# Kernel optimization log

Hardware: AMD Instinct MI355X
Metric: run time of the kernel (lower is better)

Reference implementation:

```python
import jax, jax.numpy as jnp
import numpy as np

B, T, C = 4, 2048, 1024

def setup_inputs() -> dict:
    key = jax.random.key(0)
    kx, kq, kk, kv = jax.random.split(key, 4)
    s = C ** -0.5  # match nn.Linear init scale roughly
    return {
        "x": jax.random.normal(kx, (B, T, C), dtype=jnp.float32),
        "Wq": jax.random.normal(kq, (C, C), dtype=jnp.float32) * s,
        "Wk": jax.random.normal(kk, (C, C), dtype=jnp.float32) * s,
        "Wv": jax.random.normal(kv, (C, C), dtype=jnp.float32) * s,
    }

def reference(x, Wq, Wk, Wv):
    Bq, Tq, Cq = x.shape
    # nn.Linear: y = x @ W^T (bias=False)
    q = jnp.einsum('btc,dc->btd', x, Wq)
    k = jnp.einsum('btc,dc->btd', x, Wk)
    v = jnp.einsum('btc,dc->btd', x, Wv)
    scale = Cq ** -0.5
    qk = jnp.einsum('btd,bsd->bts', q, k) * scale  # [B, T, T]
    causal = jnp.tril(jnp.ones((Tq, Tq), dtype=bool))
    qk = jnp.where(causal, qk, -jnp.inf)
    attn = jax.nn.softmax(qk, axis=-1)
    out = jnp.einsum('bts,bsd->btd', attn, v)
    return out
```

## Files before the change

kernel.cpp:

```cpp
#include <hip/hip_runtime.h>
#include <hip/hip_fp16.h>


typedef __attribute__((ext_vector_type(8))) _Float16 half8;
typedef __attribute__((ext_vector_type(4))) _Float16 half4;
typedef __attribute__((ext_vector_type(4))) float f32x4;

template<int TM, int TN, int WM, int WN, bool SWAP>
__device__ __forceinline__ void gemm_nt_core(
    const _Float16* __restrict__ A, const _Float16* __restrict__ B,
    int lda, int ldb, int k0, int k1,
    _Float16* ldsA, _Float16* ldsB,
    f32x4 acc[TM / (WM * 16)][TN / (WN * 16)])
{
    constexpr int FM = TM / (WM * 16), FN = TN / (WN * 16);
    constexpr int NA = TM / 32, NB = TN / 32;
    const int t    = threadIdx.x;
    const int lane = t & 63;
    const int w    = t >> 6;
    const int wm   = w % WM;
    const int wn   = w / WM;
    const int lr   = lane & 15;
    const int lq   = lane >> 4;

    const _Float16* ga[NA]; int loA[NA];
    const _Float16* gb[NB]; int loB[NB];
#pragma unroll
    for (int i = 0; i < NA; ++i) {
        int f = t + 256 * i;
        int r = f >> 3, c = (f & 7) ^ ((f >> 3) & 7);
        ga[i] = A + (size_t)r * lda + c * 8;
        loA[i] = f * 8;
    }
#pragma unroll
    for (int i = 0; i < NB; ++i) {
        int f = t + 256 * i;
        int r = f >> 3, c = (f & 7) ^ ((f >> 3) & 7);
        gb[i] = B + (size_t)r * ldb + c * 8;
        loB[i] = f * 8;
    }

    int offA[2][FM], offB[2][FN];
#pragma unroll
    for (int h = 0; h < 2; ++h) {
#pragma unroll
        for (int i = 0; i < FM; ++i) {
            int R = wm * (TM / WM) + i * 16 + lr;
            offA[h][i] = (8 * R + ((h * 4 + lq) ^ (R & 7))) * 8;
        }
#pragma unroll
        for (int i = 0; i < FN; ++i) {
            int R = wn * (TN / WN) + i * 16 + lr;
            offB[h][i] = (8 * R + ((h * 4 + lq) ^ (R & 7))) * 8;
        }
    }

    half8 va[NA], vb[NB];
#pragma unroll
    for (int i = 0; i < NA; ++i) va[i] = *(const half8*)(ga[i] + k0);
#pragma unroll
    for (int i = 0; i < NB; ++i) vb[i] = *(const half8*)(gb[i] + k0);

    for (int k = k0; k < k1; k += 64) {
        __syncthreads();
#pragma unroll
        for (int i = 0; i < NA; ++i) *(half8*)(ldsA + loA[i]) = va[i];
#pragma unroll
        for (int i = 0; i < NB; ++i) *(half8*)(ldsB + loB[i]) = vb[i];
        if (k + 64 < k1) {
#pragma unroll
            for (int i = 0; i < NA; ++i) va[i] = *(const half8*)(ga[i] + k + 64);
#pragma unroll
            for (int i = 0; i < NB; ++i) vb[i] = *(const half8*)(gb[i] + k + 64);
        }
        __syncthreads();

#pragma unroll
        for (int h = 0; h < 2; ++h) {
            half8 af[FM], bf[FN];
#pragma unroll
            for (int i = 0; i < FM; ++i) af[i] = *(const half8*)(ldsA + offA[h][i]);
#pragma unroll
            for (int i = 0; i < FN; ++i) bf[i] = *(const half8*)(ldsB + offB[h][i]);
#pragma unroll
            for (int mi = 0; mi < FM; ++mi)
#pragma unroll
                for (int ni = 0; ni < FN; ++ni) {
                    if constexpr (SWAP)
                        acc[mi][ni] = __builtin_amdgcn_mfma_f32_16x16x32_f16(
                            bf[ni], af[mi], acc[mi][ni], 0, 0, 0);
                    else
                        acc[mi][ni] = __builtin_amdgcn_mfma_f32_16x16x32_f16(
                            af[mi], bf[ni], acc[mi][ni], 0, 0, 0);
                }
        }
    }
}

__global__ __launch_bounds__(256) void f32tof16_k(
    const float* __restrict__ in, _Float16* __restrict__ out, int n)
{
    int i = (blockIdx.x * 256 + threadIdx.x) * 4;
    if (i < n) {
        float4 f = *(const float4*)(in + i);
        half4 h = { (_Float16)f.x, (_Float16)f.y, (_Float16)f.z, (_Float16)f.w };
        *(half4*)(out + i) = h;
    }
}

__global__ __launch_bounds__(256) void wconv_k(
    const float* __restrict__ Wq, const float* __restrict__ Wk,
    const float* __restrict__ Wv, _Float16* __restrict__ out)
{
    const float* src = (blockIdx.y == 0) ? Wq : (blockIdx.y == 1) ? Wk : Wv;
    int i = (blockIdx.x * 256 + threadIdx.x) * 4;
    float4 f = *(const float4*)(src + i);
    half4 h = { (_Float16)f.x, (_Float16)f.y, (_Float16)f.z, (_Float16)f.w };
    *(half4*)(out + (size_t)blockIdx.y * 1024 * 1024 + i) = h;
}

__global__ __launch_bounds__(256) void qkv_gemm_k(
    const _Float16* __restrict__ xh, const _Float16* __restrict__ Wh,
    _Float16* __restrict__ Q, _Float16* __restrict__ K, _Float16* __restrict__ Vt)
{
    __shared__ __align__(16) _Float16 ldsA[128 * 64];
    __shared__ __align__(16) _Float16 ldsB[128 * 64];
    const int tileM = blockIdx.x * 128;
    const int tileN = blockIdx.y * 128;
    const int z     = blockIdx.z;
    const _Float16* W = Wh + (size_t)z * 1024 * 1024;

    const int lane = threadIdx.x & 63;
    const int w    = threadIdx.x >> 6;
    const int wm = w & 1, wn = w >> 1;
    const int lr = lane & 15, lq = lane >> 4;

    if (z == 2) {
        f32x4 acc[4][4] = {};
        gemm_nt_core<128, 128, 2, 2, false>(xh + (size_t)tileM * 1024,
                                            W + (size_t)tileN * 1024,
                                            1024, 1024, 0, 1024, ldsA, ldsB, acc);
#pragma unroll
        for (int mi = 0; mi < 4; ++mi)
#pragma unroll
            for (int ni = 0; ni < 4; ++ni) {
                int m0 = tileM + wm * 64 + mi * 16 + lq * 4;
                int n  = tileN + wn * 64 + ni * 16 + lr;
                int b = m0 >> 11, tt = m0 & 2047;
                half4 h = { (_Float16)acc[mi][ni][0], (_Float16)acc[mi][ni][1],
                            (_Float16)acc[mi][ni][2], (_Float16)acc[mi][ni][3] };
                *(half4*)(Vt + (size_t)b * 2048 * 1024 + (size_t)n * 2048 + tt) = h;
            }
    } else {
        f32x4 acc[4][4] = {};
        gemm_nt_core<128, 128, 2, 2, true>(xh + (size_t)tileM * 1024,
                                           W + (size_t)tileN * 1024,
                                           1024, 1024, 0, 1024, ldsA, ldsB, acc);
        _Float16* O = (z == 0) ? Q : K;
#pragma unroll
        for (int mi = 0; mi < 4; ++mi)
#pragma unroll
            for (int ni = 0; ni < 4; ++ni) {
                int tt = tileM + wm * 64 + mi * 16 + lr;
                int d0 = tileN + wn * 64 + ni * 16 + lq * 4;
                half4 h = { (_Float16)acc[mi][ni][0], (_Float16)acc[mi][ni][1],
                            (_Float16)acc[mi][ni][2], (_Float16)acc[mi][ni][3] };
                *(half4*)(O + (size_t)tt * 1024 + d0) = h;
            }
    }
}

__global__ __launch_bounds__(256) void scores_gemm_k(
    const _Float16* __restrict__ Q, const _Float16* __restrict__ K,
    _Float16* __restrict__ S)
{
    const int ti = blockIdx.x, si = blockIdx.y;
    if (si > ti) return;
    const int tileT = ti * 128, tileS = si * 128, b = blockIdx.z;

    __shared__ __align__(16) _Float16 ldsA[128 * 64];
    __shared__ __align__(16) _Float16 ldsB[128 * 64];
    f32x4 acc[4][4] = {};
    gemm_nt_core<128, 128, 2, 2, true>(
        Q + (size_t)b * 2048 * 1024 + (size_t)tileT * 1024,
        K + (size_t)b * 2048 * 1024 + (size_t)tileS * 1024,
        1024, 1024, 0, 1024, ldsA, ldsB, acc);

    const int lane = threadIdx.x & 63;
    const int w    = threadIdx.x >> 6;
    const int wm = w & 1, wn = w >> 1;
    const int lr = lane & 15, lq = lane >> 4;
    const float scale = 0.03125f;

#pragma unroll
    for (int mi = 0; mi < 4; ++mi)
#pragma unroll
        for (int ni = 0; ni < 4; ++ni) {
            int tt = tileT + wm * 64 + mi * 16 + lr;
            int s0 = tileS + wn * 64 + ni * 16 + lq * 4;
            half4 h;
#pragma unroll
            for (int r = 0; r < 4; ++r)
                h[r] = (s0 + r <= tt) ? (_Float16)(acc[mi][ni][r] * scale)
                                      : (_Float16)0.f;
            *(half4*)(S + ((size_t)b * 2048 + tt) * 2048 + s0) = h;
        }
}

__global__ __launch_bounds__(256) void softmax_k(_Float16* __restrict__ S)
{
    const int w    = threadIdx.x >> 6;
    const int lane = threadIdx.x & 63;
    const int t    = blockIdx.x * 4 + w;
    const int b    = blockIdx.y;
    _Float16* row = S + ((size_t)b * 2048 + t) * 2048;

    float x[32];
    float mx = -1e30f;
#pragma unroll
    for (int j = 0; j < 4; ++j) {
        half8 h = *(const half8*)(row + j * 512 + lane * 8);
#pragma unroll
        for (int e = 0; e < 8; ++e) {
            int s = j * 512 + lane * 8 + e;
            float f = (s <= t) ? (float)h[e] : -1e30f;
            x[j * 8 + e] = f;
            mx = fmaxf(mx, f);
        }
    }
#pragma unroll
    for (int o = 32; o > 0; o >>= 1) mx = fmaxf(mx, __shfl_xor(mx, o));

    float sum = 0.f;
#pragma unroll
    for (int i = 0; i < 32; ++i) {
        float e = __expf(x[i] - mx);
        x[i] = e;
        sum += e;
    }
#pragma unroll
    for (int o = 32; o > 0; o >>= 1) sum += __shfl_xor(sum, o);
    const float inv = 1.0f / sum;

#pragma unroll
    for (int j = 0; j < 4; ++j) {
        half8 p;
#pragma unroll
        for (int e = 0; e < 8; ++e) p[e] = (_Float16)(x[j * 8 + e] * inv);
        *(half8*)(row + j * 512 + lane * 8) = p;
    }
}

__global__ __launch_bounds__(256) void pv_gemm_k(
    const _Float16* __restrict__ P, const _Float16* __restrict__ Vt,
    float* __restrict__ out)
{
    __shared__ __align__(16) _Float16 ldsA[128 * 64];
    __shared__ __align__(16) _Float16 ldsB[64 * 64];
    const int tileT = (15 - blockIdx.x) * 128;
    const int tileD = blockIdx.y * 64;
    const int b     = blockIdx.z;
    const int kEnd  = tileT + 128;

    f32x4 acc[4][2] = {};
    gemm_nt_core<128, 64, 2, 2, true>(
        P + ((size_t)b * 2048 + tileT) * 2048,
        Vt + (size_t)b * 1024 * 2048 + (size_t)tileD * 2048,
        2048, 2048, 0, kEnd, ldsA, ldsB, acc);

    const int lane = threadIdx.x & 63;
    const int w    = threadIdx.x >> 6;
    const int wm = w & 1, wn = w >> 1;
    const int lr = lane & 15, lq = lane >> 4;

#pragma unroll
    for (int mi = 0; mi < 4; ++mi)
#pragma unroll
        for (int ni = 0; ni < 2; ++ni) {
            int tt = tileT + wm * 64 + mi * 16 + lr;
            int d0 = tileD + wn * 32 + ni * 16 + lq * 4;
            *(f32x4*)(out + ((size_t)b * 2048 + tt) * 1024 + d0) = acc[mi][ni];
        }
}

extern "C" void kernel_launch(void* const* d_in, const int* in_sizes, int n_in,
                              void* d_out, int out_size, void* d_ws, size_t ws_size,
                              hipStream_t stream)
{
    const float* x  = (const float*)d_in[0];
    const float* Wq = (const float*)d_in[1];
    const float* Wk = (const float*)d_in[2];
    const float* Wv = (const float*)d_in[3];
    float* out = (float*)d_out;

    char* ws = (char*)d_ws;
    _Float16* xh = (_Float16*)(ws);
    _Float16* Wh = (_Float16*)(ws + (16u << 20));
    _Float16* Qh = (_Float16*)(ws + (22u << 20));
    _Float16* Kh = (_Float16*)(ws + (38u << 20));
    _Float16* Vt = (_Float16*)(ws + (54u << 20));
    _Float16* S  = (_Float16*)(ws + (70u << 20));

    f32tof16_k<<<8192, 256, 0, stream>>>(x, xh, 4 * 2048 * 1024);
    wconv_k<<<dim3(1024, 3), 256, 0, stream>>>(Wq, Wk, Wv, Wh);

    qkv_gemm_k<<<dim3(64, 8, 3), 256, 0, stream>>>(xh, Wh, Qh, Kh, Vt);

    scores_gemm_k<<<dim3(16, 16, 4), 256, 0, stream>>>(Qh, Kh, S);
    softmax_k<<<dim3(512, 4), 256, 0, stream>>>(S);
    pv_gemm_k<<<dim3(16, 16, 4), 256, 0, stream>>>(S, Vt, out);
}
```

Baseline: 266.5 us.

## Rewrite QKV projection as 256x256 pipelined GEMM with direct global-to-LDS loads

Replaces the 128x128 QKV projection GEMM with a 256x256-tile, 512-thread kernel. Operands are streamed directly into swizzled LDS with global_load_lds, double-buffered, and the MFMA work is split into four phases per k-tile interleaved with prefetches and priority hints. The aim is more reuse per tile and hiding of global memory latency behind MFMA work. The cost is 128KB of LDS per block and far fewer blocks (384). The hand-written waitcnt and barrier choreography is fragile.

Measured after the change: 267.2 us. No clear change (+0.3%).

```diff
diff --git a/kernel.cpp b/kernel.cpp
--- a/kernel.cpp
+++ b/kernel.cpp
@@ -97,6 +97,161 @@
     }
 }
 
+__device__ __forceinline__ void gload_lds16(const void* g, void* l)
+{
+    __builtin_amdgcn_global_load_lds(
+        (const __attribute__((address_space(1))) void*)g,
+        (__attribute__((address_space(3))) void*)l, 16, 0, 0);
+}
+
+template<bool SWAP>
+__device__ __forceinline__ void gemm_nt_256(
+    const _Float16* __restrict__ A, const _Float16* __restrict__ B,
+    const int lda, const int ldb, const int kTiles,
+    _Float16* lds, f32x4 acc[8][4])
+{
+    const int t    = threadIdx.x;
+    const int lane = t & 63;
+    const int w    = t >> 6;
+    const int wm   = w & 1;
+    const int wn   = w >> 1;
+    const int lr   = lane & 15;
+    const int lq   = lane >> 4;
+
+    const int r0 = t >> 3;
+    const int c0 = (t & 7) ^ (r0 & 7);
+    const _Float16* gA = A + (size_t)r0 * lda + c0 * 8;
+    const _Float16* gB = B + (size_t)r0 * ldb + c0 * 8;
+
+    char* ldsc = (char*)lds;
+    char* stA = ldsc + w * 1024;
+    char* stB = ldsc + 65536 + w * 1024;
+
+    const int x0 = ((0 + lq) ^ (lr & 7)) * 16;
+    const int x1 = ((4 + lq) ^ (lr & 7)) * 16;
+    const char* rdA = ldsc + wm * 16384 + lr * 128;
+    const char* rdB = ldsc + 65536 + (wn >> 1) * 16384 + (wn & 1) * 8192
+                      + lr * 128;
+
+    half8 af[4][2], bf0[2][2], bf1[2][2];
+
+#define STGA(BUF, H, KOFF) do {                                               \
+    const _Float16* _s = gA + (size_t)(H) * 128 * lda + (KOFF);               \
+    char* _d = stA + (BUF) * 32768 + (H) * 16384;                             \
+    gload_lds16(_s, _d);                                                      \
+    gload_lds16(_s + (size_t)64 * lda, _d + 8192);                            \
+} while (0)
+
+#define STGB(BUF, H, KOFF) do {                                               \
+    const _Float16* _s = gB + (size_t)(H) * 128 * ldb + (KOFF);               \
+    char* _d = stB + (BUF) * 32768 + (H) * 16384;                             \
+    gload_lds16(_s, _d);                                                      \
+    gload_lds16(_s + (size_t)64 * ldb, _d + 8192);                            \
+} while (0)
+
+#define LDA_Q(BUF, MQ) do {                                                   \
+    const char* _p = rdA + (BUF) * 32768 + (MQ) * 8192;                       \
+    _Pragma("unroll")                                                         \
+    for (int mi = 0; mi < 4; ++mi) {                                          \
+        af[mi][0] = *(const half8*)(_p + mi * 2048 + x0);                     \
+        af[mi][1] = *(const half8*)(_p + mi * 2048 + x1);                     \
+    }                                                                         \
+} while (0)
+
+#define LDB_Q(DST, BUF, NQ) do {                                              \
+    const char* _p = rdB + (BUF) * 32768 + (NQ) * 4096;                       \
+    _Pragma("unroll")                                                         \
+    for (int ni = 0; ni < 2; ++ni) {                                          \
+        DST[ni][0] = *(const half8*)(_p + ni * 2048 + x0);                    \
+        DST[ni][1] = *(const half8*)(_p + ni * 2048 + x1);                    \
+    }                                                                         \
+} while (0)
+
+#define MFMA_Q(MQ, NQ, BSRC) do {                                             \
+    _Pragma("unroll")                                                         \
+    for (int mi = 0; mi < 4; ++mi)                                            \
+    _Pragma("unroll")                                                         \
+    for (int ni = 0; ni < 2; ++ni)                                            \
+    _Pragma("unroll")                                                         \
+    for (int kh = 0; kh < 2; ++kh) {                                          \
+        if constexpr (SWAP)                                                   \
+            acc[(MQ)*4+mi][(NQ)*2+ni] = __builtin_amdgcn_mfma_f32_16x16x32_f16(\
+                BSRC[ni][kh], af[mi][kh], acc[(MQ)*4+mi][(NQ)*2+ni], 0, 0, 0);\
+        else                                                                  \
+            acc[(MQ)*4+mi][(NQ)*2+ni] = __builtin_amdgcn_mfma_f32_16x16x32_f16(\
+                af[mi][kh], BSRC[ni][kh], acc[(MQ)*4+mi][(NQ)*2+ni], 0, 0, 0);\
+    }                                                                         \
+} while (0)
+
+#define PH_PRE() do {                                                         \
+    asm volatile("" ::: "memory");                                            \
+    __builtin_amdgcn_s_barrier();                                             \
+    asm volatile("s_waitcnt lgkmcnt(0)" ::: "memory");                        \
+    __builtin_amdgcn_sched_barrier(0);                                        \
+    __builtin_amdgcn_s_setprio(1);                                            \
+} while (0)
+
+#define PH_POST() do {                                                        \
+    __builtin_amdgcn_s_setprio(0);                                            \
+    __builtin_amdgcn_sched_barrier(0);                                        \
+    __builtin_amdgcn_s_barrier();                                             \
+    asm volatile("" ::: "memory");                                            \
+} while (0)
+
+#define KTILE(KT, BUF) do {                                                   \
+    const int _k1 = ((KT) + 1) * 64, _k2 = ((KT) + 2) * 64;                   \
+    const bool _s1 = (KT) + 1 < kTiles, _s2 = (KT) + 2 < kTiles;              \
+                                                                      \
+    LDA_Q(BUF, 0);                                                            \
+    LDB_Q(bf0, BUF, 0);                                                       \
+    if (_s1) STGA((BUF) ^ 1, 1, _k1);                                         \
+    PH_PRE(); MFMA_Q(0, 0, bf0); PH_POST();                                   \
+                                                                      \
+    LDB_Q(bf1, BUF, 1);                                                       \
+    if (_s1) STGB((BUF) ^ 1, 1, _k1);                                         \
+    PH_PRE(); MFMA_Q(0, 1, bf1); PH_POST();                                   \
+                                                                      \
+    LDA_Q(BUF, 1);                                                            \
+    if (_s2) STGB(BUF, 0, _k2);                                               \
+    PH_PRE(); MFMA_Q(1, 1, bf1); PH_POST();                                   \
+                                     \
+    if (_s2) STGA(BUF, 0, _k2);                                               \
+    asm volatile("" ::: "memory");                                            \
+    __builtin_amdgcn_s_barrier();                                             \
+    __builtin_amdgcn_s_setprio(1);                                            \
+    MFMA_Q(1, 0, bf0);                                                        \
+    __builtin_amdgcn_s_setprio(0);                                            \
+    if (_s2) asm volatile("s_waitcnt vmcnt(4)" ::: "memory");                 \
+    else     asm volatile("s_waitcnt vmcnt(0)" ::: "memory");                 \
+    __builtin_amdgcn_sched_barrier(0);                                        \
+    __builtin_amdgcn_s_barrier();                                             \
+    asm volatile("" ::: "memory");                                            \
+} while (0)
+
+    STGA(0, 0, 0); STGA(0, 1, 0); STGB(0, 0, 0); STGB(0, 1, 0);
+    if (kTiles > 1) { STGB(1, 0, 64); STGA(1, 0, 64); }
+    if (kTiles > 1) asm volatile("s_waitcnt vmcnt(4)" ::: "memory");
+    else            asm volatile("s_waitcnt vmcnt(0)" ::: "memory");
+    __builtin_amdgcn_sched_barrier(0);
+    __builtin_amdgcn_s_barrier();
+    asm volatile("" ::: "memory");
+
+#pragma unroll 1
+    for (int kt = 0; kt < kTiles; kt += 2) {
+        KTILE(kt, 0);
+        KTILE(kt + 1, 1);
+    }
+
+#undef STGA
+#undef STGB
+#undef LDA_Q
+#undef LDB_Q
+#undef MFMA_Q
+#undef PH_PRE
+#undef PH_POST
+#undef KTILE
+}
+
 __global__ __launch_bounds__(256) void f32tof16_k(
     const float* __restrict__ in, _Float16* __restrict__ out, int n)
 {
@@ -119,14 +274,14 @@
     *(half4*)(out + (size_t)blockIdx.y * 1024 * 1024 + i) = h;
 }
 
-__global__ __launch_bounds__(256) void qkv_gemm_k(
+__global__ __launch_bounds__(512, 2) void qkv_gemm256_k(
     const _Float16* __restrict__ xh, const _Float16* __restrict__ Wh,
-    _Float16* __restrict__ Q, _Float16* __restrict__ K, _Float16* __restrict__ Vt)
-{
-    __shared__ __align__(16) _Float16 ldsA[128 * 64];
-    __shared__ __align__(16) _Float16 ldsB[128 * 64];
-    const int tileM = blockIdx.x * 128;
-    const int tileN = blockIdx.y * 128;
+    _Float16* __restrict__ Q, _Float16* __restrict__ K,
+    _Float16* __restrict__ Vt)
+{
+    __shared__ __align__(16) _Float16 lds[65536];
+    const int tileM = blockIdx.x * 256;
+    const int tileN = blockIdx.y * 256;
     const int z     = blockIdx.z;
     const _Float16* W = Wh + (size_t)z * 1024 * 1024;
 
@@ -135,16 +290,15 @@
     const int wm = w & 1, wn = w >> 1;
     const int lr = lane & 15, lq = lane >> 4;
 
+    f32x4 acc[8][4] = {};
     if (z == 2) {
-        f32x4 acc[4][4] = {};
-        gemm_nt_core<128, 128, 2, 2, false>(xh + (size_t)tileM * 1024,
-                                            W + (size_t)tileN * 1024,
-                                            1024, 1024, 0, 1024, ldsA, ldsB, acc);
-#pragma unroll
-        for (int mi = 0; mi < 4; ++mi)
+        gemm_nt_256<false>(xh + (size_t)tileM * 1024, W + (size_t)tileN * 1024,
+                           1024, 1024, 16, lds, acc);
+#pragma unroll
+        for (int mi = 0; mi < 8; ++mi)
 #pragma unroll
             for (int ni = 0; ni < 4; ++ni) {
-                int m0 = tileM + wm * 64 + mi * 16 + lq * 4;
+                int m0 = tileM + wm * 128 + mi * 16 + lq * 4;
                 int n  = tileN + wn * 64 + ni * 16 + lr;
                 int b = m0 >> 11, tt = m0 & 2047;
                 half4 h = { (_Float16)acc[mi][ni][0], (_Float16)acc[mi][ni][1],
@@ -152,16 +306,14 @@
                 *(half4*)(Vt + (size_t)b * 2048 * 1024 + (size_t)n * 2048 + tt) = h;
             }
     } else {
-        f32x4 acc[4][4] = {};
-        gemm_nt_core<128, 128, 2, 2, true>(xh + (size_t)tileM * 1024,
-                                           W + (size_t)tileN * 1024,
-                                           1024, 1024, 0, 1024, ldsA, ldsB, acc);
+        gemm_nt_256<true>(xh + (size_t)tileM * 1024, W + (size_t)tileN * 1024,
+                          1024, 1024, 16, lds, acc);
         _Float16* O = (z == 0) ? Q : K;
 #pragma unroll
-        for (int mi = 0; mi < 4; ++mi)
+        for (int mi = 0; mi < 8; ++mi)
 #pragma unroll
             for (int ni = 0; ni < 4; ++ni) {
-                int tt = tileM + wm * 64 + mi * 16 + lr;
+                int tt = tileM + wm * 128 + mi * 16 + lr;
                 int d0 = tileN + wn * 64 + ni * 16 + lq * 4;
                 half4 h = { (_Float16)acc[mi][ni][0], (_Float16)acc[mi][ni][1],
                             (_Float16)acc[mi][ni][2], (_Float16)acc[mi][ni][3] };
@@ -304,7 +456,7 @@
     f32tof16_k<<<8192, 256, 0, stream>>>(x, xh, 4 * 2048 * 1024);
     wconv_k<<<dim3(1024, 3), 256, 0, stream>>>(Wq, Wk, Wv, Wh);
 
-    qkv_gemm_k<<<dim3(64, 8, 3), 256, 0, stream>>>(xh, Wh, Qh, Kh, Vt);
+    qkv_gemm256_k<<<dim3(32, 4, 3), 512, 0, stream>>>(xh, Wh, Qh, Kh, Vt);
 
     scores_gemm_k<<<dim3(16, 16, 4), 256, 0, stream>>>(Qh, Kh, S);
     softmax_k<<<dim3(512, 4), 256, 0, stream>>>(S);
```

## Load GEMM tiles directly into LDS and skip masked softmax chunks

Applied to the files above, without the earlier changes.

Global-to-LDS tile loads in the shared GEMM core now use the direct global_load_lds path instead of staging through registers. This removes the register-prefetch double buffering, so loads are no longer overlapped with the previous tile's MFMA work. Softmax now skips loading, exponentiating and storing 512-column chunks that lie entirely past the causal boundary. Launch bounds request 4 blocks per CU for the GEMM kernels, which caps registers per thread.

New measurement: 302.4 us. +13.5%, slower.

```diff
diff --git a/kernel.cpp b/kernel.cpp
--- a/kernel.cpp
+++ b/kernel.cpp
@@ -6,73 +6,69 @@
 typedef __attribute__((ext_vector_type(4))) _Float16 half4;
 typedef __attribute__((ext_vector_type(4))) float f32x4;
 
-template<int TM, int TN, int WM, int WN, bool SWAP>
-__device__ __forceinline__ void gemm_nt_core(
+__device__ __forceinline__ void gload_lds16(const void* g, void* l)
+{
+    __builtin_amdgcn_global_load_lds(
+        (const __attribute__((address_space(1))) void*)g,
+        (__attribute__((address_space(3))) void*)l, 16, 0, 0);
+}
+
+template<int TM, int TN, bool SWAP>
+__device__ __forceinline__ void gemm_nt_gl(
     const _Float16* __restrict__ A, const _Float16* __restrict__ B,
     int lda, int ldb, int k0, int k1,
     _Float16* ldsA, _Float16* ldsB,
-    f32x4 acc[TM / (WM * 16)][TN / (WN * 16)])
-{
-    constexpr int FM = TM / (WM * 16), FN = TN / (WN * 16);
+    f32x4 acc[TM / 32][TN / 32])
+{
+    constexpr int FM = TM / 32, FN = TN / 32;
     constexpr int NA = TM / 32, NB = TN / 32;
     const int t    = threadIdx.x;
     const int lane = t & 63;
     const int w    = t >> 6;
-    const int wm   = w % WM;
-    const int wn   = w / WM;
+    const int wm   = w & 1;
+    const int wn   = w >> 1;
     const int lr   = lane & 15;
     const int lq   = lane >> 4;
 
-    const _Float16* ga[NA]; int loA[NA];
-    const _Float16* gb[NB]; int loB[NB];
+    const _Float16* ga[NA]; const _Float16* gb[NB];
 #pragma unroll
     for (int i = 0; i < NA; ++i) {
         int f = t + 256 * i;
         int r = f >> 3, c = (f & 7) ^ ((f >> 3) & 7);
         ga[i] = A + (size_t)r * lda + c * 8;
-        loA[i] = f * 8;
     }
 #pragma unroll
     for (int i = 0; i < NB; ++i) {
         int f = t + 256 * i;
         int r = f >> 3, c = (f & 7) ^ ((f >> 3) & 7);
         gb[i] = B + (size_t)r * ldb + c * 8;
-        loB[i] = f * 8;
-    }
+    }
+    char* lcA = (char*)ldsA;
+    char* lcB = (char*)ldsB;
 
     int offA[2][FM], offB[2][FN];
 #pragma unroll
     for (int h = 0; h < 2; ++h) {
 #pragma unroll
         for (int i = 0; i < FM; ++i) {
-            int R = wm * (TM / WM) + i * 16 + lr;
+            int R = wm * (TM / 2) + i * 16 + lr;
             offA[h][i] = (8 * R + ((h * 4 + lq) ^ (R & 7))) * 8;
         }
 #pragma unroll
         for (int i = 0; i < FN; ++i) {
-            int R = wn * (TN / WN) + i * 16 + lr;
+            int R = wn * (TN / 2) + i * 16 + lr;
             offB[h][i] = (8 * R + ((h * 4 + lq) ^ (R & 7))) * 8;
         }
     }
-
-    half8 va[NA], vb[NB];
-#pragma unroll
-    for (int i = 0; i < NA; ++i) va[i] = *(const half8*)(ga[i] + k0);
-#pragma unroll
-    for (int i = 0; i < NB; ++i) vb[i] = *(const half8*)(gb[i] + k0);
 
     for (int k = k0; k < k1; k += 64) {
         __syncthreads();
 #pragma unroll
-        for (int i = 0; i < NA; ++i) *(half8*)(ldsA + loA[i]) = va[i];
-#pragma unroll
-        for (int i = 0; i < NB; ++i) *(half8*)(ldsB + loB[i]) = vb[i];
-        if (k + 64 < k1) {
-#pragma unroll
-            for (int i = 0; i < NA; ++i) va[i] = *(const half8*)(ga[i] + k + 64);
-#pragma unroll
-            for (int i = 0; i < NB; ++i) vb[i] = *(const half8*)(gb[i] + k + 64);
-        }
+        for (int i = 0; i < NA; ++i)
+            gload_lds16(ga[i] + k, lcA + (t + 256 * i) * 16);
+#pragma unroll
+        for (int i = 0; i < NB; ++i)
+            gload_lds16(gb[i] + k, lcB + (t + 256 * i) * 16);
         __syncthreads();
 
 #pragma unroll
@@ -119,9 +115,10 @@
     *(half4*)(out + (size_t)blockIdx.y * 1024 * 1024 + i) = h;
 }
 
-__global__ __launch_bounds__(256) void qkv_gemm_k(
+__global__ __launch_bounds__(256, 4) void qkv_gemm_k(
     const _Float16* __restrict__ xh, const _Float16* __restrict__ Wh,
-    _Float16* __restrict__ Q, _Float16* __restrict__ K, _Float16* __restrict__ Vt)
+    _Float16* __restrict__ Q, _Float16* __restrict__ K,
+    _Float16* __restrict__ Vt)
 {
     __shared__ __align__(16) _Float16 ldsA[128 * 64];
     __shared__ __align__(16) _Float16 ldsB[128 * 64];
@@ -135,11 +132,11 @@
     const int wm = w & 1, wn = w >> 1;
     const int lr = lane & 15, lq = lane >> 4;
 
+    f32x4 acc[4][4] = {};
     if (z == 2) {
-        f32x4 acc[4][4] = {};
-        gemm_nt_core<128, 128, 2, 2, false>(xh + (size_t)tileM * 1024,
-                                            W + (size_t)tileN * 1024,
-                                            1024, 1024, 0, 1024, ldsA, ldsB, acc);
+        gemm_nt_gl<128, 128, false>(xh + (size_t)tileM * 1024,
+                                    W + (size_t)tileN * 1024,
+                                    1024, 1024, 0, 1024, ldsA, ldsB, acc);
 #pragma unroll
         for (int mi = 0; mi < 4; ++mi)
 #pragma unroll
@@ -152,10 +149,9 @@
                 *(half4*)(Vt + (size_t)b * 2048 * 1024 + (size_t)n * 2048 + tt) = h;
             }
     } else {
-        f32x4 acc[4][4] = {};
-        gemm_nt_core<128, 128, 2, 2, true>(xh + (size_t)tileM * 1024,
-                                           W + (size_t)tileN * 1024,
-                                           1024, 1024, 0, 1024, ldsA, ldsB, acc);
+        gemm_nt_gl<128, 128, true>(xh + (size_t)tileM * 1024,
+                                   W + (size_t)tileN * 1024,
+                                   1024, 1024, 0, 1024, ldsA, ldsB, acc);
         _Float16* O = (z == 0) ? Q : K;
 #pragma unroll
         for (int mi = 0; mi < 4; ++mi)
@@ -170,7 +166,7 @@
     }
 }
 
-__global__ __launch_bounds__(256) void scores_gemm_k(
+__global__ __launch_bounds__(256, 4) void scores_gemm_k(
     const _Float16* __restrict__ Q, const _Float16* __restrict__ K,
     _Float16* __restrict__ S)
 {
@@ -181,7 +177,7 @@
     __shared__ __align__(16) _Float16 ldsA[128 * 64];
     __shared__ __align__(16) _Float16 ldsB[128 * 64];
     f32x4 acc[4][4] = {};
-    gemm_nt_core<128, 128, 2, 2, true>(
+    gemm_nt_gl<128, 128, true>(
         Q + (size_t)b * 2048 * 1024 + (size_t)tileT * 1024,
         K + (size_t)b * 2048 * 1024 + (size_t)tileS * 1024,
         1024, 1024, 0, 1024, ldsA, ldsB, acc);
@@ -214,18 +210,21 @@
     const int t    = blockIdx.x * 4 + w;
     const int b    = blockIdx.y;
     _Float16* row = S + ((size_t)b * 2048 + t) * 2048;
+    const int jmax = t >> 9;
 
     float x[32];
     float mx = -1e30f;
 #pragma unroll
     for (int j = 0; j < 4; ++j) {
-        half8 h = *(const half8*)(row + j * 512 + lane * 8);
-#pragma unroll
-        for (int e = 0; e < 8; ++e) {
-            int s = j * 512 + lane * 8 + e;
-            float f = (s <= t) ? (float)h[e] : -1e30f;
-            x[j * 8 + e] = f;
-            mx = fmaxf(mx, f);
+        if (j <= jmax) {
+            half8 h = *(const half8*)(row + j * 512 + lane * 8);
+#pragma unroll
+            for (int e = 0; e < 8; ++e) {
+                int s = j * 512 + lane * 8 + e;
+                float f = (s <= t) ? (float)h[e] : -1e30f;
+                x[j * 8 + e] = f;
+                mx = fmaxf(mx, f);
+            }
         }
     }
 #pragma unroll
@@ -233,10 +232,15 @@
 
     float sum = 0.f;
 #pragma unroll
-    for (int i = 0; i < 32; ++i) {
-        float e = __expf(x[i] - mx);
-        x[i] = e;
-        sum += e;
+    for (int j = 0; j < 4; ++j) {
+        if (j <= jmax) {
+#pragma unroll
+            for (int e = 0; e < 8; ++e) {
+                float ex = __expf(x[j * 8 + e] - mx);
+                x[j * 8 + e] = ex;
+                sum += ex;
+            }
+        }
     }
 #pragma unroll
     for (int o = 32; o > 0; o >>= 1) sum += __shfl_xor(sum, o);
@@ -244,14 +248,16 @@
 
 #pragma unroll
     for (int j = 0; j < 4; ++j) {
-        half8 p;
-#pragma unroll
-        for (int e = 0; e < 8; ++e) p[e] = (_Float16)(x[j * 8 + e] * inv);
-        *(half8*)(row + j * 512 + lane * 8) = p;
-    }
-}
-
-__global__ __launch_bounds__(256) void pv_gemm_k(
+        if (j <= jmax) {
+            half8 p;
+#pragma unroll
+            for (int e = 0; e < 8; ++e) p[e] = (_Float16)(x[j * 8 + e] * inv);
+            *(half8*)(row + j * 512 + lane * 8) = p;
+        }
+    }
+}
+
+__global__ __launch_bounds__(256, 4) void pv_gemm_k(
     const _Float16* __restrict__ P, const _Float16* __restrict__ Vt,
     float* __restrict__ out)
 {
@@ -263,7 +269,7 @@
     const int kEnd  = tileT + 128;
 
     f32x4 acc[4][2] = {};
-    gemm_nt_core<128, 64, 2, 2, true>(
+    gemm_nt_gl<128, 64, true>(
         P + ((size_t)b * 2048 + tileT) * 2048,
         Vt + (size_t)b * 1024 * 2048 + (size_t)tileD * 2048,
         2048, 2048, 0, kEnd, ldsA, ldsB, acc);
```
